# Optimization experiments

Hardware: AMD Instinct MI355X
Metric: run time of the kernel (lower is better)

Reference implementation:

```python
import jax, jax.numpy as jnp
import numpy as np

# ---- fixed problem dims (match init_kwargs) ----
B = 256            # graph pairs
NQ, NC = 96, 120   # nodes per query / corpus graph
EQ, EC = 192, 240  # edges per query / corpus graph
M = 256            # max_edge_set_size (pad target)
RAW = 32           # raw node/edge feature dim
H = 64             # node_state_dim
MSG = 128          # message_dim == encoded edge dim
SDIM = 64          # sinkhorn_feature_dim
PROP_STEPS = 3
TIME_STEPS = 2
SINK_ITERS = 10
TEMP = 0.1
N_NODES = B * (NQ + NC)
N_EDGES = B * (EQ + EC)


def _mlp2(x, W1, b1, W2, b2):
    return jax.nn.relu(x @ W1 + b1) @ W2 + b2


def _split_and_stack(ef):
    # edges laid out [q0, c0, q1, c1, ...]; pad each graph's edges to M
    D = ef.shape[-1]
    ef = ef.reshape(B, EQ + EC, D)
    q = jnp.pad(ef[:, :EQ], ((0, 0), (0, M - EQ), (0, 0)))
    c = jnp.pad(ef[:, EQ:], ((0, 0), (0, M - EC), (0, 0)))
    return q, c


def _sinkhorn(log_alpha):
    la = log_alpha / TEMP
    for _ in range(SINK_ITERS):
        la = la - jax.nn.logsumexp(la, axis=2, keepdims=True)
        la = la - jax.nn.logsumexp(la, axis=1, keepdims=True)
    return jnp.exp(la)


def setup_inputs() -> dict:
    key = jax.random.key(0)
    ks = jax.random.split(key, 16)
    rng = np.random.default_rng(0)
    nodes_per_graph = np.tile(np.array([NQ, NC]), B)            # [2B]
    node_offsets = np.concatenate([[0], np.cumsum(nodes_per_graph)[:-1]])
    edges_per_graph = np.tile(np.array([EQ, EC]), B)
    eg = np.repeat(np.arange(2 * B), edges_per_graph)           # graph id per edge
    from_idx = node_offsets[eg] + rng.integers(0, nodes_per_graph[eg])
    to_idx = node_offsets[eg] + rng.integers(0, nodes_per_graph[eg])

    def lin(k, i, o):
        return (jax.random.normal(k, (i, o), jnp.float32) / np.sqrt(i)).astype(jnp.float32)

    return {
        "node_features": jax.random.normal(ks[0], (N_NODES, RAW), jnp.float32),
        "edge_features": jax.random.normal(ks[1], (N_EDGES, RAW), jnp.float32),
        "from_idx": jnp.asarray(from_idx, jnp.int32),
        "to_idx": jnp.asarray(to_idx, jnp.int32),
        "enc_node_W": lin(ks[2], RAW, H), "enc_node_b": jnp.zeros((H,), jnp.float32),
        "enc_edge_W": lin(ks[3], RAW, MSG), "enc_edge_b": jnp.zeros((MSG,), jnp.float32),
        "msg_W1": lin(ks[4], 2 * H + MSG, 2 * MSG), "msg_b1": jnp.zeros((2 * MSG,), jnp.float32),
        "msg_W2": lin(ks[5], 2 * MSG, MSG), "msg_b2": jnp.zeros((MSG,), jnp.float32),
        "upd_W1": lin(ks[6], H + 2 * MSG, 2 * H), "upd_b1": jnp.zeros((2 * H,), jnp.float32),
        "upd_W2": lin(ks[7], 2 * H, H), "upd_b2": jnp.zeros((H,), jnp.float32),
        "int_W1": lin(ks[8], 2 * MSG, 2 * MSG), "int_b1": jnp.zeros((2 * MSG,), jnp.float32),
        "int_W2": lin(ks[9], 2 * MSG, MSG), "int_b2": jnp.zeros((MSG,), jnp.float32),
        "sink_W1": lin(ks[10], MSG, SDIM), "sink_b1": jnp.zeros((SDIM,), jnp.float32),
        "sink_W2": lin(ks[11], SDIM, SDIM), "sink_b2": jnp.zeros((SDIM,), jnp.float32),
    }


def _forward(node_features, edge_features,
             enc_node_W, enc_node_b, enc_edge_W, enc_edge_b,
             msg_W1, msg_b1, msg_W2, msg_b2,
             upd_W1, upd_b1, upd_W2, upd_b2,
             int_W1, int_b1, int_W2, int_b2,
             sink_W1, sink_b1, sink_W2, sink_b2,
             from_idx, to_idx):
    h0 = node_features @ enc_node_W + enc_node_b      # GraphEncoder (nodes)
    e0 = edge_features @ enc_edge_W + enc_edge_b      # GraphEncoder (edges) -> MSG dim
    mask_q = (jnp.arange(M) < EQ).astype(h0.dtype)[None, :, None]
    mask_c = (jnp.arange(M) < EC).astype(h0.dtype)[None, :, None]

    def edge_msgs(h, comb):
        hf, ht = h[from_idx], h[to_idx]
        mf = _mlp2(jnp.concatenate([hf, ht, comb], -1), msg_W1, msg_b1, msg_W2, msg_b2)
        mb = _mlp2(jnp.concatenate([ht, hf, comb], -1), msg_W1, msg_b1, msg_W2, msg_b2)
        return mf, mb

    plan = None
    q_store = c_store = None
    for _ in range(TIME_STEPS):
        h, e = h0, e0
        inter = jnp.zeros((N_EDGES, MSG), e0.dtype)
        for _ in range(PROP_STEPS):
            # interaction encoder on [edge_features_enc, interaction_features]
            comb = _mlp2(jnp.concatenate([e, inter], -1), int_W1, int_b1, int_W2, int_b2)
            # prop_layer: bidirectional messages + aggregation + node update
            mf, mb = edge_msgs(h, comb)
            agg_f = jax.ops.segment_sum(mf, to_idx, num_segments=N_NODES)
            agg_b = jax.ops.segment_sum(mb, from_idx, num_segments=N_NODES)
            h = _mlp2(jnp.concatenate([h, agg_f, agg_b], -1), upd_W1, upd_b1, upd_W2, upd_b2)
            # propagation_messages: per-edge messages from updated node states
            mf2, mb2 = edge_msgs(h, comb)
            e = mf2 + mb2
            # interaction features via transport-plan gather (zeros on first time step)
            if plan is None:
                inter = jnp.zeros((N_EDGES, MSG), e.dtype)
            else:
                qs, cs = _split_and_stack(e)
                q_int = jnp.einsum('bqc,bcd->bqd', plan, cs)[:, :EQ]
                c_int = jnp.einsum('bqc,bqd->bcd', plan, qs)[:, :EC]
                inter = jnp.concatenate([q_int, c_int], 1).reshape(N_EDGES, MSG)
        q_store, c_store = _split_and_stack(e)
        fq = _mlp2(q_store, sink_W1, sink_b1, sink_W2, sink_b2) * mask_q
        fc = _mlp2(c_store, sink_W1, sink_b1, sink_W2, sink_b2) * mask_c
        plan = _sinkhorn(jnp.einsum('bqd,bcd->bqc', fq, fc))
    # feature_alignment_score: -||Q - P C||_1 per pair
    return -jnp.abs(q_store - jnp.einsum('bqc,bcd->bqd', plan, c_store)).sum((1, 2))


def reference(node_features, edge_features, from_idx, to_idx,
              enc_node_W, enc_node_b, enc_edge_W, enc_edge_b,
              msg_W1, msg_b1, msg_W2, msg_b2,
              upd_W1, upd_b1, upd_W2, upd_b2,
              int_W1, int_b1, int_W2, int_b2,
              sink_W1, sink_b1, sink_W2, sink_b2):
    return _forward(node_features, edge_features,
                    enc_node_W, enc_node_b, enc_edge_W, enc_edge_b,
                    msg_W1, msg_b1, msg_W2, msg_b2,
                    upd_W1, upd_b1, upd_W2, upd_b2,
                    int_W1, int_b1, int_W2, int_b2,
                    sink_W1, sink_b1, sink_W2, sink_b2,
                    from_idx, to_idx)
```

## Files before the change

### kernel.cpp

```cpp
#include <hip/hip_runtime.h>
#include <math.h>

constexpr int BATCH = 256;
constexpr int EQ_   = 192;
constexpr int EC_   = 240;
constexpr int EPG   = 432;
constexpr int NPG   = 216;
constexpr int NN    = BATCH * NPG;
constexpr int NE    = BATCH * EPG;

typedef __attribute__((ext_vector_type(8))) short short8;
typedef __attribute__((ext_vector_type(4))) float floatx4;
typedef unsigned short u16;

__device__ __forceinline__ u16 f2bf(float x) {
  union { float f; unsigned u; } c; c.f = x;
  const unsigned r = (c.u + 0x7FFFu + ((c.u >> 16) & 1u)) >> 16;
  return (u16)r;
}
__device__ __forceinline__ float bf2f(u16 x) {
  union { unsigned u; float f; } c; c.u = ((unsigned)x) << 16;
  return c.f;
}
__device__ __forceinline__ unsigned pack2(float a, float b) {
  return (unsigned)f2bf(a) | ((unsigned)f2bf(b) << 16);
}
__device__ __forceinline__ short8 cvt8(const float* __restrict__ p) {
  const float4 a = *(const float4*)p;
  const float4 b = *(const float4*)(p + 4);
  short8 o;
  o[0]=(short)f2bf(a.x); o[1]=(short)f2bf(a.y); o[2]=(short)f2bf(a.z); o[3]=(short)f2bf(a.w);
  o[4]=(short)f2bf(b.x); o[5]=(short)f2bf(b.y); o[6]=(short)f2bf(b.z); o[7]=(short)f2bf(b.w);
  return o;
}

__device__ __forceinline__ void lse_online(float& m, float& s, float tt) {
  if (tt > m) { s = s * __expf(m - tt) + 1.f; m = tt; }
  else        { s += __expf(tt - m); }
}

__global__ __launch_bounds__(256)
void wconv(const float* __restrict__ W, u16* __restrict__ out, int K, int N)
{
  const int i = blockIdx.x * 256 + threadIdx.x;
  if (i < K * N) {
    const int n = i / K, k = i - n * K;
    out[i] = f2bf(W[(size_t)k * N + n]);
  }
}

__global__ __launch_bounds__(256)
void wconv_split(const float* __restrict__ W, u16* __restrict__ hi,
                 u16* __restrict__ lo, int K, int N)
{
  const int i = blockIdx.x * 256 + threadIdx.x;
  if (i < K * N) {
    const int n = i / K, k = i - n * K;
    const float w = W[(size_t)k * N + n];
    const u16 h = f2bf(w);
    hi[i] = h;
    lo[i] = f2bf(w - bf2f(h));
  }
}

template<int K1, int HID, int NOUT, int IN_MODE, int DUAL, int OUT_MODE, int WAVES>
__global__ __launch_bounds__(WAVES * 64, 4)
void mlp_mfma(const void* __restrict__ X, const void* __restrict__ P2,
              const void* __restrict__ P3, const u16* __restrict__ CB,
              const int* __restrict__ IA, const int* __restrict__ IB,
              const u16* __restrict__ W1t, const float* __restrict__ B1,
              const u16* __restrict__ W2t, const float* __restrict__ B2,
              float* __restrict__ Yf, u16* __restrict__ Yb0, u16* __restrict__ Yb1)
{
  constexpr int RT  = 32;
  constexpr int THREADS = WAVES * 64;
  constexpr int KCH = K1 / 8;
  constexpr int NT1 = HID / (WAVES * 16);
  constexpr int NT2 = (NOUT / (WAVES * 16) > 0) ? NOUT / (WAVES * 16) : 1;
  constexpr int SAB = RT * K1 * 2;
  constexpr int SHB = RT * (HID + 8) * 2;
  __shared__ __align__(16) char smem[(SAB > SHB ? SAB : SHB)];
  u16* sA = (u16*)smem;
  u16* sH = (u16*)smem;

  const int tid = threadIdx.x;
  const int rowBase = blockIdx.x * RT;

  for (int ch = tid; ch < RT * KCH; ch += THREADS) {
    const int r = ch / KCH, kc = ch - r * KCH;
    const int gr = rowBase + r, k0 = kc * 8;
    short8 pk;
    if constexpr (IN_MODE == 4) {
      const float* Xf  = (const float*)X;
      const float* P2f = (const float*)P2;
      if (k0 < 128)      pk = cvt8(&Xf[(size_t)gr * 128 + k0]);
      else if (P2f)      pk = cvt8(&P2f[(size_t)gr * 128 + (k0 - 128)]);
      else { pk = short8{0,0,0,0,0,0,0,0}; }
    } else if constexpr (IN_MODE == 1) {
      const u16* Hb = (const u16*)X;
      if (k0 < 64)       pk = *(const short8*)&Hb[(size_t)IA[gr] * 64 + k0];
      else if (k0 < 128) pk = *(const short8*)&Hb[(size_t)IB[gr] * 64 + (k0 - 64)];
      else               pk = *(const short8*)&CB[(size_t)gr * 128 + (k0 - 128)];
    } else {
      const u16* Hb = (const u16*)X;
      const u16* A0 = (const u16*)P2;
      const u16* A1 = (const u16*)P3;
      if (k0 < 64)       pk = *(const short8*)&Hb[(size_t)gr * 64 + k0];
      else if (k0 < 192) pk = *(const short8*)&A0[(size_t)gr * 128 + (k0 - 64)];
      else               pk = *(const short8*)&A1[(size_t)gr * 128 + (k0 - 192)];
    }
    const int byte = ((r * K1 + k0) * 2) ^ ((r & 7) << 4);
    *(short8*)((char*)sA + byte) = pk;
  }
  __syncthreads();

  const int wid = tid >> 6, lane = tid & 63;
  const int l15 = lane & 15, lg = lane >> 4;

  floatx4 acc1[1 + DUAL][2][NT1];
  #pragma unroll
  for (int d = 0; d <= DUAL; ++d)
    #pragma unroll
    for (int m = 0; m < 2; ++m)
      #pragma unroll
      for (int n = 0; n < NT1; ++n) acc1[d][m][n] = floatx4{0.f,0.f,0.f,0.f};

  #pragma unroll 2
  for (int kk = 0; kk < K1 / 32; ++kk) {
    short8 bw[NT1];
    #pragma unroll
    for (int n = 0; n < NT1; ++n) {
      const int col = wid * (HID / WAVES) + n * 16 + l15;
      bw[n] = *(const short8*)&W1t[(size_t)col * K1 + kk * 32 + lg * 8];
    }
    #pragma unroll
    for (int d = 0; d <= DUAL; ++d) {
      int k0 = kk * 32 + lg * 8;
      if (DUAL && d && k0 < 128) k0 ^= 64;
      #pragma unroll
      for (int m = 0; m < 2; ++m) {
        const int r = m * 16 + l15;
        const int byte = ((r * K1 + k0) * 2) ^ ((r & 7) << 4);
        const short8 af = *(const short8*)((char*)sA + byte);
        #pragma unroll
        for (int n = 0; n < NT1; ++n)
          acc1[d][m][n] = __builtin_amdgcn_mfma_f32_16x16x32_bf16(af, bw[n], acc1[d][m][n], 0, 0, 0);
      }
    }
  }
  __syncthreads();

  floatx4 accO[2][NT2];
  #pragma unroll
  for (int m = 0; m < 2; ++m)
    #pragma unroll
    for (int n = 0; n < NT2; ++n) accO[m][n] = floatx4{0.f,0.f,0.f,0.f};

  #pragma unroll
  for (int d = 0; d <= DUAL; ++d) {
    #pragma unroll
    for (int n = 0; n < NT1; ++n) {
      const int col = wid * (HID / WAVES) + n * 16 + l15;
      const float b1 = B1[col];
      #pragma unroll
      for (int m = 0; m < 2; ++m)
        #pragma unroll
        for (int r = 0; r < 4; ++r) {
          const int row = m * 16 + lg * 4 + r;
          const float y = acc1[d][m][n][r] + b1;
          sH[row * (HID + 8) + col] = f2bf(y > 0.f ? y : 0.f);
        }
    }
    __syncthreads();
    if (OUT_MODE == 2 && d == 1) {
      #pragma unroll
      for (int m = 0; m < 2; ++m)
        #pragma unroll
        for (int n = 0; n < NT2; ++n) accO[m][n] = floatx4{0.f,0.f,0.f,0.f};
    }
    #pragma unroll 2
    for (int kk = 0; kk < HID / 32; ++kk) {
      short8 bw2[NT2];
      #pragma unroll
      for (int n = 0; n < NT2; ++n) {
        const int col = wid * (NOUT / WAVES) + n * 16 + l15;
        bw2[n] = *(const short8*)&W2t[(size_t)col * HID + kk * 32 + lg * 8];
      }
      #pragma unroll
      for (int m = 0; m < 2; ++m) {
        const short8 af = *(const short8*)&sH[(m * 16 + l15) * (HID + 8) + kk * 32 + lg * 8];
        #pragma unroll
        for (int n = 0; n < NT2; ++n)
          accO[m][n] = __builtin_amdgcn_mfma_f32_16x16x32_bf16(af, bw2[n], accO[m][n], 0, 0, 0);
      }
    }
    if constexpr (OUT_MODE == 2) {
      u16* Y = d ? Yb1 : Yb0;
      #pragma unroll
      for (int n = 0; n < NT2; ++n) {
        const int col = wid * (NOUT / WAVES) + n * 16 + l15;
        const float b2 = B2[col];
        #pragma unroll
        for (int m = 0; m < 2; ++m)
          #pragma unroll
          for (int r = 0; r < 4; ++r) {
            const int gr = rowBase + m * 16 + lg * 4 + r;
            Y[(size_t)gr * NOUT + col] = f2bf(accO[m][n][r] + b2);
          }
      }
    }
    if (DUAL && d == 0) __syncthreads();
  }

  if constexpr (OUT_MODE != 2) {
    #pragma unroll
    for (int n = 0; n < NT2; ++n) {
      const int col = wid * (NOUT / WAVES) + n * 16 + l15;
      const float b2 = B2[col] * (float)(1 + DUAL);
      #pragma unroll
      for (int m = 0; m < 2; ++m)
        #pragma unroll
        for (int r = 0; r < 4; ++r) {
          const int gr = rowBase + m * 16 + lg * 4 + r;
          const float y = accO[m][n][r] + b2;
          if constexpr (OUT_MODE == 1) {
            Yb0[(size_t)gr * NOUT + col] = f2bf(y);
          } else {
            Yf[(size_t)gr * NOUT + col] = y;
            if constexpr (OUT_MODE == 3)
              Yb0[(size_t)gr * NOUT + col] = f2bf(y);
          }
        }
    }
  }
}

template<int EBF16>
__global__ __launch_bounds__(512, 4)
void comb_msg_fused(const void* __restrict__ E, const u16* __restrict__ INTER,
                    const u16* __restrict__ Hb,
                    const int* __restrict__ IA, const int* __restrict__ IB,
                    const u16* __restrict__ Wi1, const float* __restrict__ Bi1,
                    const u16* __restrict__ Wi2, const float* __restrict__ Bi2,
                    const u16* __restrict__ Wm1, const float* __restrict__ Bm1,
                    const u16* __restrict__ Wm2, const float* __restrict__ Bm2,
                    u16* __restrict__ COMB, u16* __restrict__ MI)
{
  constexpr int RT = 32;
  __shared__ __align__(16) char smem[RT * (256 + 8) * 2];
  u16* sA = (u16*)smem;
  u16* sH = (u16*)smem;

  const int tid = threadIdx.x;
  const int rowBase = blockIdx.x * RT;
  const int wid = tid >> 6, lane = tid & 63;
  const int l15 = lane & 15, lg = lane >> 4;

  for (int ch = tid; ch < RT * 32; ch += 512) {
    const int r = ch >> 5, kc = ch & 31;
    const int gr = rowBase + r, k0 = kc * 8;
    short8 pk;
    if (k0 < 128) {
      if constexpr (EBF16) pk = *(const short8*)&((const u16*)E)[(size_t)gr * 128 + k0];
      else                 pk = cvt8(&((const float*)E)[(size_t)gr * 128 + k0]);
    }
    else if (INTER) pk = *(const short8*)&INTER[(size_t)gr * 128 + (k0 - 128)];
    else            pk = short8{0,0,0,0,0,0,0,0};
    const int byte = ((r * 256 + k0) * 2) ^ ((r & 7) << 4);
    *(short8*)((char*)sA + byte) = pk;
  }
  __syncthreads();

  floatx4 c1[2][2];
  #pragma unroll
  for (int m = 0; m < 2; ++m) { c1[m][0] = floatx4{0,0,0,0}; c1[m][1] = floatx4{0,0,0,0}; }
  #pragma unroll 2
  for (int kk = 0; kk < 8; ++kk) {
    short8 bw[2];
    #pragma unroll
    for (int n = 0; n < 2; ++n) {
      const int col = wid * 32 + n * 16 + l15;
      bw[n] = *(const short8*)&Wi1[(size_t)col * 256 + kk * 32 + lg * 8];
    }
    #pragma unroll
    for (int m = 0; m < 2; ++m) {
      const int r = m * 16 + l15;
      const int byte = ((r * 256 + kk * 32 + lg * 8) * 2) ^ ((r & 7) << 4);
      const short8 af = *(const short8*)((char*)sA + byte);
      c1[m][0] = __builtin_amdgcn_mfma_f32_16x16x32_bf16(af, bw[0], c1[m][0], 0, 0, 0);
      c1[m][1] = __builtin_amdgcn_mfma_f32_16x16x32_bf16(af, bw[1], c1[m][1], 0, 0, 0);
    }
  }
  __syncthreads();
  #pragma unroll
  for (int n = 0; n < 2; ++n) {
    const int col = wid * 32 + n * 16 + l15;
    const float b1 = Bi1[col];
    #pragma unroll
    for (int m = 0; m < 2; ++m)
      #pragma unroll
      for (int r = 0; r < 4; ++r) {
        const int row = m * 16 + lg * 4 + r;
        const float y = c1[m][n][r] + b1;
        sH[row * 264 + col] = f2bf(y > 0.f ? y : 0.f);
      }
  }
  __syncthreads();
  floatx4 cO[2];
  cO[0] = floatx4{0,0,0,0}; cO[1] = floatx4{0,0,0,0};
  #pragma unroll 2
  for (int kk = 0; kk < 8; ++kk) {
    const int col = wid * 16 + l15;
    const short8 bw2 = *(const short8*)&Wi2[(size_t)col * 256 + kk * 32 + lg * 8];
    #pragma unroll
    for (int m = 0; m < 2; ++m) {
      const short8 af = *(const short8*)&sH[(m * 16 + l15) * 264 + kk * 32 + lg * 8];
      cO[m] = __builtin_amdgcn_mfma_f32_16x16x32_bf16(af, bw2, cO[m], 0, 0, 0);
    }
  }
  __syncthreads();

  {
    const int col = wid * 16 + l15;
    const float b2 = Bi2[col];
    #pragma unroll
    for (int m = 0; m < 2; ++m)
      #pragma unroll
      for (int r = 0; r < 4; ++r) {
        const int row = m * 16 + lg * 4 + r;
        const int gr = rowBase + row;
        const u16 v = f2bf(cO[m][r] + b2);
        COMB[(size_t)gr * 128 + col] = v;
        const int k0 = 128 + col;
        const int byte = ((row * 256 + k0) * 2) ^ ((row & 7) << 4);
        *(u16*)((char*)sA + byte) = v;
      }
  }
  for (int ch = tid; ch < RT * 16; ch += 512) {
    const int r = ch >> 4, kc = ch & 15;
    const int gr = rowBase + r, k0 = kc * 8;
    short8 pk;
    if (k0 < 64) pk = *(const short8*)&Hb[(size_t)IA[gr] * 64 + k0];
    else         pk = *(const short8*)&Hb[(size_t)IB[gr] * 64 + (k0 - 64)];
    const int byte = ((r * 256 + k0) * 2) ^ ((r & 7) << 4);
    *(short8*)((char*)sA + byte) = pk;
  }
  __syncthreads();

  floatx4 m1[2][2][2];
  #pragma unroll
  for (int d = 0; d < 2; ++d)
    #pragma unroll
    for (int m = 0; m < 2; ++m) { m1[d][m][0] = floatx4{0,0,0,0}; m1[d][m][1] = floatx4{0,0,0,0}; }
  #pragma unroll 2
  for (int kk = 0; kk < 8; ++kk) {
    short8 bw[2];
    #pragma unroll
    for (int n = 0; n < 2; ++n) {
      const int col = wid * 32 + n * 16 + l15;
      bw[n] = *(const short8*)&Wm1[(size_t)col * 256 + kk * 32 + lg * 8];
    }
    #pragma unroll
    for (int d = 0; d < 2; ++d) {
      int k0 = kk * 32 + lg * 8;
      if (d && k0 < 128) k0 ^= 64;
      #pragma unroll
      for (int m = 0; m < 2; ++m) {
        const int r = m * 16 + l15;
        const int byte = ((r * 256 + k0) * 2) ^ ((r & 7) << 4);
        const short8 af = *(const short8*)((char*)sA + byte);
        m1[d][m][0] = __builtin_amdgcn_mfma_f32_16x16x32_bf16(af, bw[0], m1[d][m][0], 0, 0, 0);
        m1[d][m][1] = __builtin_amdgcn_mfma_f32_16x16x32_bf16(af, bw[1], m1[d][m][1], 0, 0, 0);
      }
    }
  }
  __syncthreads();

  floatx4 mO[2];
  #pragma unroll
  for (int d = 0; d < 2; ++d) {
    #pragma unroll
    for (int n = 0; n < 2; ++n) {
      const int col = wid * 32 + n * 16 + l15;
      const float b1 = Bm1[col];
      #pragma unroll
      for (int m = 0; m < 2; ++m)
        #pragma unroll
        for (int r = 0; r < 4; ++r) {
          const int row = m * 16 + lg * 4 + r;
          const float y = m1[d][m][n][r] + b1;
          sH[row * 264 + col] = f2bf(y > 0.f ? y : 0.f);
        }
    }
    __syncthreads();
    mO[0] = floatx4{0,0,0,0}; mO[1] = floatx4{0,0,0,0};
    #pragma unroll 2
    for (int kk = 0; kk < 8; ++kk) {
      const int col = wid * 16 + l15;
      const short8 bw2 = *(const short8*)&Wm2[(size_t)col * 256 + kk * 32 + lg * 8];
      #pragma unroll
      for (int m = 0; m < 2; ++m) {
        const short8 af = *(const short8*)&sH[(m * 16 + l15) * 264 + kk * 32 + lg * 8];
        mO[m] = __builtin_amdgcn_mfma_f32_16x16x32_bf16(af, bw2, mO[m], 0, 0, 0);
      }
    }
    {
      const int col = wid * 16 + l15;
      const float b2 = Bm2[col];
      #pragma unroll
      for (int m = 0; m < 2; ++m)
        #pragma unroll
        for (int r = 0; r < 4; ++r) {
          const int gr = rowBase + m * 16 + lg * 4 + r;
          MI[(size_t)gr * 256 + d * 128 + col] = f2bf(mO[m][r] + b2);
        }
    }
    if (d == 0) __syncthreads();
  }
}

__global__ __launch_bounds__(512)
void scatter_agg(const u16* __restrict__ MI,
                 const int* __restrict__ FI, const int* __restrict__ TI,
                 u16* __restrict__ AggF, u16* __restrict__ AggB)
{
  const int pair = blockIdx.x >> 1, dir = blockIdx.x & 1;
  const int* SI = dir ? FI : TI;
  u16* Agg      = dir ? AggB : AggF;
  const int tid = threadIdx.x;
  __shared__ float sAgg[NPG * 128];

  for (int i = tid; i < NPG * 128; i += 512) sAgg[i] = 0.f;
  __syncthreads();

  for (int i = tid; i < EPG * 32; i += 512) {
    const int edge = i >> 5, cb = i & 31;
    const int er = pair * EPG + edge;
    const int node = SI[er] - pair * NPG;
    const size_t base = (size_t)er * 256 + dir * 128 + cb;
    #pragma unroll
    for (int k = 0; k < 4; ++k)
      atomicAdd(&sAgg[node * 128 + cb + 32 * k], bf2f(MI[base + 32 * k]));
  }
  __syncthreads();
  unsigned* dst = (unsigned*)(Agg + (size_t)pair * NPG * 128);
  for (int i = tid; i < NPG * 64; i += 512)
    dst[i] = pack2(sAgg[2 * i], sAgg[2 * i + 1]);
}

template<int K1, int HID, int NOUT, int IN_MODE, int SINGLE, int OUTBF>
__global__ __launch_bounds__(256)
void fused_mlp(const float* __restrict__ X, const float* __restrict__ P1,
               const float* __restrict__ W1, const float* __restrict__ B1,
               const float* __restrict__ W2, const float* __restrict__ B2,
               float* __restrict__ Y, u16* __restrict__ Yb, int maskLen)
{
  constexpr int RT = 32, BK = 32;
  constexpr int J1 = HID / 32;
  constexpr int J2 = NOUT / 32;
  constexpr int BMAX = (HID > NOUT ? HID : NOUT);
  __shared__ float sA[RT * 33];
  __shared__ float sB[BK * BMAX];
  __shared__ float sH[SINGLE ? 1 : RT * (HID + 1)];

  const int t  = threadIdx.x;
  const int tx = t & 31, ty = t >> 5;
  const int rowBase = blockIdx.x * RT;

  float acc[4][J1];
  #pragma unroll
  for (int i = 0; i < 4; ++i)
    #pragma unroll
    for (int j = 0; j < J1; ++j) acc[i][j] = 0.f;

  for (int kb = 0; kb < K1; kb += BK) {
    for (int l = t; l < RT * BK; l += 256) {
      const int r = l >> 5, k = l & 31;
      const int gr = rowBase + r, gk = kb + k;
      float v;
      if constexpr (IN_MODE == 0) {
        v = X[(size_t)gr * K1 + gk];
      } else {
        const int bb = gr >> 8, m = gr & 255;
        constexpr int off = (IN_MODE == 5) ? 0 : EQ_;
        constexpr int len = (IN_MODE == 5) ? EQ_ : EC_;
        v = (m < len) ? P1[((size_t)bb * EPG + off + m) * 128 + gk] : 0.f;
      }
      sA[r * 33 + k] = v;
    }
    for (int l = t * 4; l < BK * HID; l += 1024) {
      *(float4*)&sB[l] = *(const float4*)&W1[(size_t)(kb + l / HID) * HID + (l % HID)];
    }
    __syncthreads();
    #pragma unroll
    for (int k = 0; k < BK; ++k) {
      const float a0 = sA[(ty*4+0)*33+k], a1 = sA[(ty*4+1)*33+k],
                  a2 = sA[(ty*4+2)*33+k], a3 = sA[(ty*4+3)*33+k];
      #pragma unroll
      for (int j = 0; j < J1; ++j) {
        const float bb = sB[k * HID + tx + 32*j];
        acc[0][j] += a0 * bb; acc[1][j] += a1 * bb;
        acc[2][j] += a2 * bb; acc[3][j] += a3 * bb;
      }
    }
    __syncthreads();
  }

  if constexpr (SINGLE) {
    #pragma unroll
    for (int j = 0; j < J1; ++j) {
      const int col = tx + 32*j;
      const float bias = B1[col];
      #pragma unroll
      for (int i = 0; i < 4; ++i) {
        const int gr = rowBase + ty*4 + i;
        if constexpr (OUTBF) Yb[(size_t)gr * HID + col] = f2bf(acc[i][j] + bias);
        else                 Y[(size_t)gr * HID + col] = acc[i][j] + bias;
      }
    }
  }
}

template<int OFFSET, int LEN>
__global__ __launch_bounds__(256)
void sink_mlp_split(const float* __restrict__ E,
                    const u16* __restrict__ W1hi, const u16* __restrict__ W1lo,
                    const float* __restrict__ B1,
                    const u16* __restrict__ W2hi, const u16* __restrict__ W2lo,
                    const float* __restrict__ B2,
                    float* __restrict__ Y)
{
  __shared__ u16 sAhi[32 * 136], sAlo[32 * 136];
  __shared__ u16 sHhi[32 * 72],  sHlo[32 * 72];
  const int tid = threadIdx.x;
  const int rowBase = blockIdx.x * 32;

  for (int ch = tid; ch < 32 * 16; ch += 256) {
    const int r = ch >> 4, kc = ch & 15;
    const int gr = rowBase + r, k0 = kc * 8;
    const int b = gr >> 8, m = gr & 255;
    short8 hi, lo;
    if (m < LEN) {
      const float* src = &E[((size_t)b * EPG + OFFSET + m) * 128 + k0];
      #pragma unroll
      for (int j = 0; j < 8; ++j) {
        const float v = src[j];
        const u16 h = f2bf(v);
        hi[j] = (short)h;
        lo[j] = (short)f2bf(v - bf2f(h));
      }
    } else {
      hi = short8{0,0,0,0,0,0,0,0};
      lo = short8{0,0,0,0,0,0,0,0};
    }
    *(short8*)&sAhi[r * 136 + k0] = hi;
    *(short8*)&sAlo[r * 136 + k0] = lo;
  }
  __syncthreads();

  const int wid = tid >> 6, lane = tid & 63;
  const int l15 = lane & 15, lg = lane >> 4;
  const int col = wid * 16 + l15;

  floatx4 acc[2];
  acc[0] = floatx4{0,0,0,0}; acc[1] = floatx4{0,0,0,0};
  #pragma unroll
  for (int kk = 0; kk < 4; ++kk) {
    const short8 bh = *(const short8*)&W1hi[(size_t)col * 128 + kk * 32 + lg * 8];
    const short8 bl = *(const short8*)&W1lo[(size_t)col * 128 + kk * 32 + lg * 8];
    #pragma unroll
    for (int m = 0; m < 2; ++m) {
      const int r = m * 16 + l15;
      const short8 ahi = *(const short8*)&sAhi[r * 136 + kk * 32 + lg * 8];
      const short8 alo = *(const short8*)&sAlo[r * 136 + kk * 32 + lg * 8];
      acc[m] = __builtin_amdgcn_mfma_f32_16x16x32_bf16(ahi, bh, acc[m], 0, 0, 0);
      acc[m] = __builtin_amdgcn_mfma_f32_16x16x32_bf16(ahi, bl, acc[m], 0, 0, 0);
      acc[m] = __builtin_amdgcn_mfma_f32_16x16x32_bf16(alo, bh, acc[m], 0, 0, 0);
    }
  }
  {
    const float b1 = B1[col];
    #pragma unroll
    for (int m = 0; m < 2; ++m)
      #pragma unroll
      for (int r4 = 0; r4 < 4; ++r4) {
        const int row = m * 16 + lg * 4 + r4;
        float y = acc[m][r4] + b1;
        y = y > 0.f ? y : 0.f;
        const u16 h = f2bf(y);
        sHhi[row * 72 + col] = h;
        sHlo[row * 72 + col] = f2bf(y - bf2f(h));
      }
  }
  __syncthreads();
  floatx4 acc2[2];
  acc2[0] = floatx4{0,0,0,0}; acc2[1] = floatx4{0,0,0,0};
  #pragma unroll
  for (int kk = 0; kk < 2; ++kk) {
    const short8 bh = *(const short8*)&W2hi[(size_t)col * 64 + kk * 32 + lg * 8];
    const short8 bl = *(const short8*)&W2lo[(size_t)col * 64 + kk * 32 + lg * 8];
    #pragma unroll
    for (int m = 0; m < 2; ++m) {
      const int r = m * 16 + l15;
      const short8 ahi = *(const short8*)&sHhi[r * 72 + kk * 32 + lg * 8];
      const short8 alo = *(const short8*)&sHlo[r * 72 + kk * 32 + lg * 8];
      acc2[m] = __builtin_amdgcn_mfma_f32_16x16x32_bf16(ahi, bh, acc2[m], 0, 0, 0);
      acc2[m] = __builtin_amdgcn_mfma_f32_16x16x32_bf16(ahi, bl, acc2[m], 0, 0, 0);
      acc2[m] = __builtin_amdgcn_mfma_f32_16x16x32_bf16(alo, bh, acc2[m], 0, 0, 0);
    }
  }
  {
    const float b2 = B2[col];
    #pragma unroll
    for (int m = 0; m < 2; ++m)
      #pragma unroll
      for (int r4 = 0; r4 < 4; ++r4) {
        const int gr = rowBase + m * 16 + lg * 4 + r4;
        float y = acc2[m][r4] + b2;
        if ((gr & 255) >= LEN) y = 0.f;
        Y[(size_t)gr * 64 + col] = y;
      }
  }
}

__global__ __launch_bounds__(256)
void gemm_nt_scale(const float* __restrict__ A, const float* __restrict__ Bm,
                   float* __restrict__ C, float scale)
{
  const int b = blockIdx.z, qt = blockIdx.x, ct = blockIdx.y;
  __shared__ float sA[64 * 68];
  __shared__ float sB[64 * 68];
  const int t = threadIdx.x;
  const int tx = t & 15, ty = t >> 4;
  const float* Ab = A  + (size_t)b * 16384 + (size_t)qt * 4096;
  const float* Bb = Bm + (size_t)b * 16384 + (size_t)ct * 4096;
  for (int l = t * 4; l < 64 * 64; l += 1024) {
    const int r = l >> 6, d = l & 63;
    *(float4*)&sA[r*68 + d] = *(const float4*)&Ab[r*64 + d];
    *(float4*)&sB[r*68 + d] = *(const float4*)&Bb[r*64 + d];
  }
  __syncthreads();
  float acc[4][4] = {};
  #pragma unroll
  for (int d = 0; d < 64; ++d) {
    float a[4], bb[4];
    #pragma unroll
    for (int i = 0; i < 4; ++i) a[i]  = sA[(ty*4+i)*68 + d];
    #pragma unroll
    for (int j = 0; j < 4; ++j) bb[j] = sB[(tx+16*j)*68 + d];
    #pragma unroll
    for (int i = 0; i < 4; ++i)
      #pragma unroll
      for (int j = 0; j < 4; ++j) acc[i][j] += a[i] * bb[j];
  }
  float* Cb = C + (size_t)b * 65536 + (size_t)(qt*64) * 256 + ct*64;
  #pragma unroll
  for (int i = 0; i < 4; ++i)
    #pragma unroll
    for (int j = 0; j < 4; ++j)
      Cb[(ty*4+i)*256 + tx + 16*j] = acc[i][j] * scale;
}

template<int TRANSA, int EBF16, int OUTBF>
__global__ __launch_bounds__(256)
void gemm_plan_mfma(const float* __restrict__ P, const void* __restrict__ E,
                    void* __restrict__ Y, int RPB, int YOFF, int VOFF,
                    int VLEN, int maskRows)
{
  __shared__ u16 sP[64 * 40];
  __shared__ u16 sVT[128 * 40];
  const int b = blockIdx.y, rt = blockIdx.x;
  const int t = threadIdx.x;
  const int wid = t >> 6, lane = t & 63;
  const int l15 = lane & 15, lg = lane >> 4;
  const float* Pb = P + (size_t)b * 65536;

  floatx4 acc[8];
  #pragma unroll
  for (int n = 0; n < 8; ++n) acc[n] = floatx4{0.f,0.f,0.f,0.f};

  for (int kb = 0; kb < 256; kb += 32) {
    if constexpr (TRANSA == 0) {
      for (int l = t; l < 64 * 32; l += 256) {
        const int r = l >> 5, k = l & 31;
        sP[r * 40 + k] = f2bf(Pb[(size_t)(rt * 64 + r) * 256 + kb + k]);
      }
    } else {
      for (int l = t; l < 64 * 32; l += 256) {
        const int q = l >> 6, c = l & 63;
        sP[c * 40 + q] = f2bf(Pb[(size_t)(kb + q) * 256 + rt * 64 + c]);
      }
    }
    for (int l = t; l < 32 * 128; l += 256) {
      const int k = l >> 7, d = l & 127;
      const int vr = kb + k;
      u16 v = 0;
      if (vr < VLEN) {
        if constexpr (EBF16) v = ((const u16*)E)[((size_t)b * EPG + VOFF + vr) * 128 + d];
        else                 v = f2bf(((const float*)E)[((size_t)b * EPG + VOFF + vr) * 128 + d]);
      }
      sVT[d * 40 + k] = v;
    }
    __syncthreads();
    const short8 af = *(const short8*)&sP[(wid * 16 + l15) * 40 + lg * 8];
    #pragma unroll
    for (int n = 0; n < 8; ++n) {
      const short8 bw = *(const short8*)&sVT[(n * 16 + l15) * 40 + lg * 8];
      acc[n] = __builtin_amdgcn_mfma_f32_16x16x32_bf16(af, bw, acc[n], 0, 0, 0);
    }
    __syncthreads();
  }
  #pragma unroll
  for (int n = 0; n < 8; ++n) {
    const int col = n * 16 + l15;
    #pragma unroll
    for (int r = 0; r < 4; ++r) {
      const int row = rt * 64 + wid * 16 + lg * 4 + r;
      if (row < maskRows) {
        const size_t idx = ((size_t)b * RPB + YOFF + row) * 128 + col;
        if constexpr (OUTBF) ((u16*)Y)[idx] = f2bf(acc[n][r]);
        else                 ((float*)Y)[idx] = acc[n][r];
      }
    }
  }
}

__global__ __launch_bounds__(1024)
void sinkhorn_fused(float* __restrict__ S)
{
  const int b = blockIdx.x, t = threadIdx.x;
  float* Sb = S + (size_t)b * 65536;
  const int w = t >> 6, lane = t & 63;
  const int cbase = lane * 4;
  __shared__ float ps[16 * 256];
  __shared__ float su[256], sv[256];
  if (t < 256) sv[t] = 0.f;
  __syncthreads();

  for (int it = 0; it < 10; ++it) {
    const float4 v4 = *(const float4*)&sv[cbase];
    float4 cs = {0.f, 0.f, 0.f, 0.f};
    #pragma unroll 2
    for (int i = 0; i < 16; ++i) {
      const int r = w * 16 + i;
      const float4 s4 = *(const float4*)&Sb[(size_t)r * 256 + cbase];
      const float ax = s4.x + v4.x, ay = s4.y + v4.y;
      const float az = s4.z + v4.z, aw = s4.w + v4.w;
      float m = fmaxf(fmaxf(ax, ay), fmaxf(az, aw));
      #pragma unroll
      for (int off = 32; off; off >>= 1) m = fmaxf(m, __shfl_xor(m, off));
      float s = __expf(ax - m) + __expf(ay - m) + __expf(az - m) + __expf(aw - m);
      #pragma unroll
      for (int off = 32; off; off >>= 1) s += __shfl_xor(s, off);
      const float u = -(m + __logf(s));
      if (lane == 0) su[r] = u;
      cs.x += __expf(s4.x + u);
      cs.y += __expf(s4.y + u);
      cs.z += __expf(s4.z + u);
      cs.w += __expf(s4.w + u);
    }
    *(float4*)&ps[w * 256 + cbase] = cs;
    __syncthreads();
    if (t < 256) {
      float s = 0.f;
      #pragma unroll
      for (int k = 0; k < 16; ++k) s += ps[k * 256 + t];
      sv[t] = -__logf(fmaxf(s, 1e-38f));
    }
    __syncthreads();
  }
  for (int i = t; i < 16384; i += 1024) {
    const int row = i >> 6, c4 = (i & 63) * 4;
    float4 s4 = *(float4*)&Sb[(size_t)row * 256 + c4];
    const float uu = su[row];
    const float4 v4 = *(const float4*)&sv[c4];
    s4.x = __expf(s4.x + uu + v4.x);
    s4.y = __expf(s4.y + uu + v4.y);
    s4.z = __expf(s4.z + uu + v4.z);
    s4.w = __expf(s4.w + uu + v4.w);
    *(float4*)&Sb[(size_t)row * 256 + c4] = s4;
  }
}

__global__ __launch_bounds__(256)
void escore_kernel(const float* __restrict__ e, const float* __restrict__ pc,
                   float* __restrict__ out)
{
  const int b = blockIdx.x, t = threadIdx.x;
  float acc = 0.f;
  for (int i4 = t; i4 < 8192; i4 += 256) {
    const int flat = i4 * 4;
    const int m = flat >> 7, d = flat & 127;
    float4 p = *(const float4*)&pc[((size_t)b * 256 + m) * 128 + d];
    float4 q = {0.f, 0.f, 0.f, 0.f};
    if (m < EQ_) q = *(const float4*)&e[((size_t)b * EPG + m) * 128 + d];
    acc += fabsf(q.x - p.x) + fabsf(q.y - p.y) + fabsf(q.z - p.z) + fabsf(q.w - p.w);
  }
  __shared__ float red[256];
  red[t] = acc; __syncthreads();
  for (int s2 = 128; s2 > 0; s2 >>= 1) { if (t < s2) red[t] += red[t + s2]; __syncthreads(); }
  if (t == 0) out[b] = -red[0];
}

extern "C" void kernel_launch(void* const* d_in, const int* in_sizes, int n_in,
                              void* d_out, int out_size, void* d_ws, size_t ws_size,
                              hipStream_t stream)
{
  const float* node_features = (const float*)d_in[0];
  const float* edge_features = (const float*)d_in[1];
  const int*   from_idx      = (const int*)d_in[2];
  const int*   to_idx        = (const int*)d_in[3];
  const float* enc_node_W = (const float*)d_in[4];
  const float* enc_node_b = (const float*)d_in[5];
  const float* enc_edge_W = (const float*)d_in[6];
  const float* enc_edge_b = (const float*)d_in[7];
  const float* msg_W1 = (const float*)d_in[8];
  const float* msg_b1 = (const float*)d_in[9];
  const float* msg_W2 = (const float*)d_in[10];
  const float* msg_b2 = (const float*)d_in[11];
  const float* upd_W1 = (const float*)d_in[12];
  const float* upd_b1 = (const float*)d_in[13];
  const float* upd_W2 = (const float*)d_in[14];
  const float* upd_b2 = (const float*)d_in[15];
  const float* int_W1 = (const float*)d_in[16];
  const float* int_b1 = (const float*)d_in[17];
  const float* int_W2 = (const float*)d_in[18];
  const float* int_b2 = (const float*)d_in[19];
  const float* sink_W1 = (const float*)d_in[20];
  const float* sink_b1 = (const float*)d_in[21];
  const float* sink_W2 = (const float*)d_in[22];
  const float* sink_b2 = (const float*)d_in[23];
  float* out = (float*)d_out;

  u16* wsu = (u16*)d_ws;
  u16*   hb  = wsu;
  float* e   = (float*)(wsu + (size_t)NN * 64);
  float* shr = e + (size_t)NE * 128;
  float* S   = shr + (size_t)BATCH * 32768;
  u16* comb  = (u16*)(S + (size_t)BATCH * 65536);
  u16* e1b   = comb + (size_t)NE * 128;
  u16* h1b   = e1b + (size_t)NE * 128;
  u16* wi1 = h1b + (size_t)NN * 64;
  u16* wi2 = wi1 + 65536;
  u16* wm1 = wi2 + 32768;
  u16* wm2 = wm1 + 65536;
  u16* wu1 = wm2 + 32768;
  u16* wu2 = wu1 + 40960;
  u16* ws1h = wu2 + 8192;
  u16* ws1l = ws1h + 8192;
  u16* ws2h = ws1l + 8192;
  u16* ws2l = ws2h + 4096;

  u16* mI = (u16*)e;
  u16* interb = (u16*)shr;
  u16* aggFb  = (u16*)shr;
  u16* aggBb  = aggFb + (size_t)NN * 128;
  float* fq   = shr;
  float* fc   = shr + (size_t)BATCH * 16384;
  float* pc   = shr;

  wconv<<<256, 256, 0, stream>>>(int_W1, wi1, 256, 256);
  wconv<<<128, 256, 0, stream>>>(int_W2, wi2, 256, 128);
  wconv<<<256, 256, 0, stream>>>(msg_W1, wm1, 256, 256);
  wconv<<<128, 256, 0, stream>>>(msg_W2, wm2, 256, 128);
  wconv<<<160, 256, 0, stream>>>(upd_W1, wu1, 320, 128);
  wconv<<< 32, 256, 0, stream>>>(upd_W2, wu2, 128, 64);
  wconv_split<<<32, 256, 0, stream>>>(sink_W1, ws1h, ws1l, 128, 64);
  wconv_split<<<16, 256, 0, stream>>>(sink_W2, ws2h, ws2l, 64, 64);

  fused_mlp<32,64,64,0,1,1><<<NN/32, 256, 0, stream>>>(
      node_features, nullptr, enc_node_W, enc_node_b, nullptr, nullptr,
      nullptr, hb, -1);
  fused_mlp<32,128,128,0,1,0><<<NE/32, 256, 0, stream>>>(
      edge_features, nullptr, enc_edge_W, enc_edge_b, nullptr, nullptr,
      e, nullptr, -1);

  for (int p = 0; p < 3; ++p) {
    comb_msg_fused<0><<<NE/32, 512, 0, stream>>>(
        e, nullptr, hb, from_idx, to_idx,
        wi1, int_b1, wi2, int_b2, wm1, msg_b1, wm2, msg_b2, comb, mI);
    scatter_agg<<<BATCH*2, 512, 0, stream>>>(mI, from_idx, to_idx, aggFb, aggBb);
    mlp_mfma<320,128,64,3,0,1,4><<<NN/32, 256, 0, stream>>>(
        hb, aggFb, aggBb, nullptr, nullptr, nullptr,
        wu1, upd_b1, wu2, upd_b2, nullptr, hb, nullptr);
    if (p == 0) {
      hipMemcpyAsync(h1b, hb, (size_t)NN * 64 * 2, hipMemcpyDeviceToDevice, stream);
      mlp_mfma<256,256,128,1,1,3,8><<<NE/32, 512, 0, stream>>>(
          hb, nullptr, nullptr, comb, from_idx, to_idx,
          wm1, msg_b1, wm2, msg_b2, e, e1b, nullptr);
    } else {
      mlp_mfma<256,256,128,1,1,0,8><<<NE/32, 512, 0, stream>>>(
          hb, nullptr, nullptr, comb, from_idx, to_idx,
          wm1, msg_b1, wm2, msg_b2, e, nullptr, nullptr);
    }
  }
  sink_mlp_split<0,   EQ_><<<BATCH*8, 256, 0, stream>>>(
      e, ws1h, ws1l, sink_b1, ws2h, ws2l, sink_b2, fq);
  sink_mlp_split<EQ_, EC_><<<BATCH*8, 256, 0, stream>>>(
      e, ws1h, ws1l, sink_b1, ws2h, ws2l, sink_b2, fc);
  gemm_nt_scale<<<dim3(4,4,BATCH), 256, 0, stream>>>(fq, fc, S, 10.0f);
  sinkhorn_fused<<<BATCH, 1024, 0, stream>>>(S);

  hipMemcpyAsync(hb, h1b, (size_t)NN * 64 * 2, hipMemcpyDeviceToDevice, stream);
  gemm_plan_mfma<0,1,1><<<dim3(4, BATCH), 256, 0, stream>>>(
      S, e1b, interb, EPG, 0,   EQ_, EC_, EQ_);
  gemm_plan_mfma<1,1,1><<<dim3(4, BATCH), 256, 0, stream>>>(
      S, e1b, interb, EPG, EQ_, 0,   EQ_, EC_);

  comb_msg_fused<1><<<NE/32, 512, 0, stream>>>(
      e1b, interb, hb, from_idx, to_idx,
      wi1, int_b1, wi2, int_b2, wm1, msg_b1, wm2, msg_b2, comb, mI);
  scatter_agg<<<BATCH*2, 512, 0, stream>>>(mI, from_idx, to_idx, aggFb, aggBb);
  mlp_mfma<320,128,64,3,0,1,4><<<NN/32, 256, 0, stream>>>(
      hb, aggFb, aggBb, nullptr, nullptr, nullptr,
      wu1, upd_b1, wu2, upd_b2, nullptr, hb, nullptr);
  mlp_mfma<256,256,128,1,1,0,8><<<NE/32, 512, 0, stream>>>(
      hb, nullptr, nullptr, comb, from_idx, to_idx,
      wm1, msg_b1, wm2, msg_b2, e, nullptr, nullptr);
  gemm_plan_mfma<0,0,1><<<dim3(4, BATCH), 256, 0, stream>>>(
      S, e, interb, EPG, 0,   EQ_, EC_, EQ_);
  gemm_plan_mfma<1,0,1><<<dim3(4, BATCH), 256, 0, stream>>>(
      S, e, interb, EPG, EQ_, 0,   EQ_, EC_);

  comb_msg_fused<0><<<NE/32, 512, 0, stream>>>(
      e, interb, hb, from_idx, to_idx,
      wi1, int_b1, wi2, int_b2, wm1, msg_b1, wm2, msg_b2, comb, mI);
  scatter_agg<<<BATCH*2, 512, 0, stream>>>(mI, from_idx, to_idx, aggFb, aggBb);
  mlp_mfma<320,128,64,3,0,1,4><<<NN/32, 256, 0, stream>>>(
      hb, aggFb, aggBb, nullptr, nullptr, nullptr,
      wu1, upd_b1, wu2, upd_b2, nullptr, hb, nullptr);
  mlp_mfma<256,256,128,1,1,0,8><<<NE/32, 512, 0, stream>>>(
      hb, nullptr, nullptr, comb, from_idx, to_idx,
      wm1, msg_b1, wm2, msg_b2, e, nullptr, nullptr);

  sink_mlp_split<0,   EQ_><<<BATCH*8, 256, 0, stream>>>(
      e, ws1h, ws1l, sink_b1, ws2h, ws2l, sink_b2, fq);
  sink_mlp_split<EQ_, EC_><<<BATCH*8, 256, 0, stream>>>(
      e, ws1h, ws1l, sink_b1, ws2h, ws2l, sink_b2, fc);
  gemm_nt_scale<<<dim3(4,4,BATCH), 256, 0, stream>>>(fq, fc, S, 10.0f);
  sinkhorn_fused<<<BATCH, 1024, 0, stream>>>(S);

  gemm_plan_mfma<0,0,0><<<dim3(4, BATCH), 256, 0, stream>>>(
      S, e, pc, 256, 0, EQ_, EC_, 256);
  escore_kernel<<<BATCH, 256, 0, stream>>>(e, pc, out);
}
```

Baseline: 3.271 ms.

## Split scatter aggregation by channel half, use split-bf16 MFMA for score GEMM, bf16 edge encoder

The scatter aggregation kernel now splits each direction's 128 channels into two 64-channel halves across separate blocks. That halves shared memory per block, with padding to reduce bank conflicts, and doubles the block count for better occupancy. The fp32 FMA score GEMM is replaced by a bf16 hi/lo split MFMA version that keeps near-fp32 accuracy on matrix cores. The edge encoder now writes bf16 directly into e1b, and the first propagation step reads that bf16 buffer, which cuts fp32 traffic. The split-bf16 product drops the lo*lo term, a small precision risk. Unused code in fused_mlp is removed.

```diff
diff --git a/kernel.cpp b/kernel.cpp
--- a/kernel.cpp
+++ b/kernel.cpp
@@ -424,28 +424,30 @@
                  const int* __restrict__ FI, const int* __restrict__ TI,
                  u16* __restrict__ AggF, u16* __restrict__ AggB)
 {
-  const int pair = blockIdx.x >> 1, dir = blockIdx.x & 1;
+  const int pair = blockIdx.x >> 2, dir = (blockIdx.x >> 1) & 1, half = blockIdx.x & 1;
   const int* SI = dir ? FI : TI;
   u16* Agg      = dir ? AggB : AggF;
   const int tid = threadIdx.x;
-  __shared__ float sAgg[NPG * 128];
-
-  for (int i = tid; i < NPG * 128; i += 512) sAgg[i] = 0.f;
-  __syncthreads();
-
-  for (int i = tid; i < EPG * 32; i += 512) {
-    const int edge = i >> 5, cb = i & 31;
+  __shared__ float sAgg[NPG * 65];
+
+  for (int i = tid; i < NPG * 65; i += 512) sAgg[i] = 0.f;
+  __syncthreads();
+
+  for (int i = tid; i < EPG * 16; i += 512) {
+    const int edge = i >> 4, c0 = i & 15;
     const int er = pair * EPG + edge;
     const int node = SI[er] - pair * NPG;
-    const size_t base = (size_t)er * 256 + dir * 128 + cb;
+    const size_t base = (size_t)er * 256 + dir * 128 + half * 64 + c0;
     #pragma unroll
     for (int k = 0; k < 4; ++k)
-      atomicAdd(&sAgg[node * 128 + cb + 32 * k], bf2f(MI[base + 32 * k]));
-  }
-  __syncthreads();
-  unsigned* dst = (unsigned*)(Agg + (size_t)pair * NPG * 128);
-  for (int i = tid; i < NPG * 64; i += 512)
-    dst[i] = pack2(sAgg[2 * i], sAgg[2 * i + 1]);
+      atomicAdd(&sAgg[node * 65 + c0 + 16 * k], bf2f(MI[base + 16 * k]));
+  }
+  __syncthreads();
+  for (int i = tid; i < NPG * 32; i += 512) {
+    const int node = i >> 5, cp = i & 31;
+    unsigned* dst = (unsigned*)(Agg + (size_t)(pair * NPG + node) * 128 + half * 64);
+    dst[cp] = pack2(sAgg[node * 65 + 2 * cp], sAgg[node * 65 + 2 * cp + 1]);
+  }
 }
 
 template<int K1, int HID, int NOUT, int IN_MODE, int SINGLE, int OUTBF>
@@ -457,11 +459,9 @@
 {
   constexpr int RT = 32, BK = 32;
   constexpr int J1 = HID / 32;
-  constexpr int J2 = NOUT / 32;
-  constexpr int BMAX = (HID > NOUT ? HID : NOUT);
+  constexpr int BMAX = HID;
   __shared__ float sA[RT * 33];
   __shared__ float sB[BK * BMAX];
-  __shared__ float sH[SINGLE ? 1 : RT * (HID + 1)];
 
   const int t  = threadIdx.x;
   const int tx = t & 31, ty = t >> 5;
@@ -477,15 +477,7 @@
     for (int l = t; l < RT * BK; l += 256) {
       const int r = l >> 5, k = l & 31;
       const int gr = rowBase + r, gk = kb + k;
-      float v;
-      if constexpr (IN_MODE == 0) {
-        v = X[(size_t)gr * K1 + gk];
-      } else {
-        const int bb = gr >> 8, m = gr & 255;
-        constexpr int off = (IN_MODE == 5) ? 0 : EQ_;
-        constexpr int len = (IN_MODE == 5) ? EQ_ : EC_;
-        v = (m < len) ? P1[((size_t)bb * EPG + off + m) * 128 + gk] : 0.f;
-      }
+      float v = X[(size_t)gr * K1 + gk];
       sA[r * 33 + k] = v;
     }
     for (int l = t * 4; l < BK * HID; l += 1024) {
@@ -506,17 +498,15 @@
     __syncthreads();
   }
 
-  if constexpr (SINGLE) {
-    #pragma unroll
-    for (int j = 0; j < J1; ++j) {
-      const int col = tx + 32*j;
-      const float bias = B1[col];
-      #pragma unroll
-      for (int i = 0; i < 4; ++i) {
-        const int gr = rowBase + ty*4 + i;
-        if constexpr (OUTBF) Yb[(size_t)gr * HID + col] = f2bf(acc[i][j] + bias);
-        else                 Y[(size_t)gr * HID + col] = acc[i][j] + bias;
-      }
+  #pragma unroll
+  for (int j = 0; j < J1; ++j) {
+    const int col = tx + 32*j;
+    const float bias = B1[col];
+    #pragma unroll
+    for (int i = 0; i < 4; ++i) {
+      const int gr = rowBase + ty*4 + i;
+      if constexpr (OUTBF) Yb[(size_t)gr * HID + col] = f2bf(acc[i][j] + bias);
+      else                 Y[(size_t)gr * HID + col] = acc[i][j] + bias;
     }
   }
 }
@@ -624,41 +614,59 @@
 }
 
 __global__ __launch_bounds__(256)
-void gemm_nt_scale(const float* __restrict__ A, const float* __restrict__ Bm,
+void gemm_nt_split(const float* __restrict__ A, const float* __restrict__ Bm,
                    float* __restrict__ C, float scale)
 {
+  __shared__ u16 sQh[64 * 72], sQl[64 * 72];
+  __shared__ u16 sCh[64 * 72], sCl[64 * 72];
   const int b = blockIdx.z, qt = blockIdx.x, ct = blockIdx.y;
-  __shared__ float sA[64 * 68];
-  __shared__ float sB[64 * 68];
   const int t = threadIdx.x;
-  const int tx = t & 15, ty = t >> 4;
   const float* Ab = A  + (size_t)b * 16384 + (size_t)qt * 4096;
   const float* Bb = Bm + (size_t)b * 16384 + (size_t)ct * 4096;
-  for (int l = t * 4; l < 64 * 64; l += 1024) {
-    const int r = l >> 6, d = l & 63;
-    *(float4*)&sA[r*68 + d] = *(const float4*)&Ab[r*64 + d];
-    *(float4*)&sB[r*68 + d] = *(const float4*)&Bb[r*64 + d];
-  }
-  __syncthreads();
-  float acc[4][4] = {};
-  #pragma unroll
-  for (int d = 0; d < 64; ++d) {
-    float a[4], bb[4];
-    #pragma unroll
-    for (int i = 0; i < 4; ++i) a[i]  = sA[(ty*4+i)*68 + d];
-    #pragma unroll
-    for (int j = 0; j < 4; ++j) bb[j] = sB[(tx+16*j)*68 + d];
-    #pragma unroll
-    for (int i = 0; i < 4; ++i)
-      #pragma unroll
-      for (int j = 0; j < 4; ++j) acc[i][j] += a[i] * bb[j];
-  }
-  float* Cb = C + (size_t)b * 65536 + (size_t)(qt*64) * 256 + ct*64;
-  #pragma unroll
-  for (int i = 0; i < 4; ++i)
-    #pragma unroll
-    for (int j = 0; j < 4; ++j)
-      Cb[(ty*4+i)*256 + tx + 16*j] = acc[i][j] * scale;
+
+  for (int i = t; i < 64 * 64; i += 256) {
+    const int r = i >> 6, d = i & 63;
+    float v = Ab[r * 64 + d];
+    u16 h = f2bf(v);
+    sQh[r * 72 + d] = h;
+    sQl[r * 72 + d] = f2bf(v - bf2f(h));
+    v = Bb[r * 64 + d];
+    h = f2bf(v);
+    sCh[r * 72 + d] = h;
+    sCl[r * 72 + d] = f2bf(v - bf2f(h));
+  }
+  __syncthreads();
+
+  const int wid = t >> 6, lane = t & 63;
+  const int l15 = lane & 15, lg = lane >> 4;
+
+  floatx4 acc[4];
+  #pragma unroll
+  for (int n = 0; n < 4; ++n) acc[n] = floatx4{0.f,0.f,0.f,0.f};
+
+  #pragma unroll
+  for (int kk = 0; kk < 2; ++kk) {
+    const short8 ahi = *(const short8*)&sQh[(wid * 16 + l15) * 72 + kk * 32 + lg * 8];
+    const short8 alo = *(const short8*)&sQl[(wid * 16 + l15) * 72 + kk * 32 + lg * 8];
+    #pragma unroll
+    for (int n = 0; n < 4; ++n) {
+      const short8 bh = *(const short8*)&sCh[(n * 16 + l15) * 72 + kk * 32 + lg * 8];
+      const short8 bl = *(const short8*)&sCl[(n * 16 + l15) * 72 + kk * 32 + lg * 8];
+      acc[n] = __builtin_amdgcn_mfma_f32_16x16x32_bf16(ahi, bh, acc[n], 0, 0, 0);
+      acc[n] = __builtin_amdgcn_mfma_f32_16x16x32_bf16(ahi, bl, acc[n], 0, 0, 0);
+      acc[n] = __builtin_amdgcn_mfma_f32_16x16x32_bf16(alo, bh, acc[n], 0, 0, 0);
+    }
+  }
+  float* Cb = C + (size_t)b * 65536;
+  #pragma unroll
+  for (int n = 0; n < 4; ++n) {
+    const int col = ct * 64 + n * 16 + l15;
+    #pragma unroll
+    for (int r4 = 0; r4 < 4; ++r4) {
+      const int row = qt * 64 + wid * 16 + lg * 4 + r4;
+      Cb[(size_t)row * 256 + col] = acc[n][r4] * scale;
+    }
+  }
 }
 
 template<int TRANSA, int EBF16, int OUTBF>
@@ -871,15 +879,20 @@
   fused_mlp<32,64,64,0,1,1><<<NN/32, 256, 0, stream>>>(
       node_features, nullptr, enc_node_W, enc_node_b, nullptr, nullptr,
       nullptr, hb, -1);
-  fused_mlp<32,128,128,0,1,0><<<NE/32, 256, 0, stream>>>(
+  fused_mlp<32,128,128,0,1,1><<<NE/32, 256, 0, stream>>>(
       edge_features, nullptr, enc_edge_W, enc_edge_b, nullptr, nullptr,
-      e, nullptr, -1);
+      nullptr, e1b, -1);
 
   for (int p = 0; p < 3; ++p) {
-    comb_msg_fused<0><<<NE/32, 512, 0, stream>>>(
-        e, nullptr, hb, from_idx, to_idx,
-        wi1, int_b1, wi2, int_b2, wm1, msg_b1, wm2, msg_b2, comb, mI);
-    scatter_agg<<<BATCH*2, 512, 0, stream>>>(mI, from_idx, to_idx, aggFb, aggBb);
+    if (p == 0)
+      comb_msg_fused<1><<<NE/32, 512, 0, stream>>>(
+          e1b, nullptr, hb, from_idx, to_idx,
+          wi1, int_b1, wi2, int_b2, wm1, msg_b1, wm2, msg_b2, comb, mI);
+    else
+      comb_msg_fused<0><<<NE/32, 512, 0, stream>>>(
+          e, nullptr, hb, from_idx, to_idx,
+          wi1, int_b1, wi2, int_b2, wm1, msg_b1, wm2, msg_b2, comb, mI);
+    scatter_agg<<<BATCH*4, 512, 0, stream>>>(mI, from_idx, to_idx, aggFb, aggBb);
     mlp_mfma<320,128,64,3,0,1,4><<<NN/32, 256, 0, stream>>>(
         hb, aggFb, aggBb, nullptr, nullptr, nullptr,
         wu1, upd_b1, wu2, upd_b2, nullptr, hb, nullptr);
@@ -898,7 +911,7 @@
       e, ws1h, ws1l, sink_b1, ws2h, ws2l, sink_b2, fq);
   sink_mlp_split<EQ_, EC_><<<BATCH*8, 256, 0, stream>>>(
       e, ws1h, ws1l, sink_b1, ws2h, ws2l, sink_b2, fc);
-  gemm_nt_scale<<<dim3(4,4,BATCH), 256, 0, stream>>>(fq, fc, S, 10.0f);
+  gemm_nt_split<<<dim3(4,4,BATCH), 256, 0, stream>>>(fq, fc, S, 10.0f);
   sinkhorn_fused<<<BATCH, 1024, 0, stream>>>(S);
 
   hipMemcpyAsync(hb, h1b, (size_t)NN * 64 * 2, hipMemcpyDeviceToDevice, stream);
@@ -910,7 +923,7 @@
   comb_msg_fused<1><<<NE/32, 512, 0, stream>>>(
       e1b, interb, hb, from_idx, to_idx,
       wi1, int_b1, wi2, int_b2, wm1, msg_b1, wm2, msg_b2, comb, mI);
-  scatter_agg<<<BATCH*2, 512, 0, stream>>>(mI, from_idx, to_idx, aggFb, aggBb);
+  scatter_agg<<<BATCH*4, 512, 0, stream>>>(mI, from_idx, to_idx, aggFb, aggBb);
   mlp_mfma<320,128,64,3,0,1,4><<<NN/32, 256, 0, stream>>>(
       hb, aggFb, aggBb, nullptr, nullptr, nullptr,
       wu1, upd_b1, wu2, upd_b2, nullptr, hb, nullptr);
@@ -925,7 +938,7 @@
   comb_msg_fused<0><<<NE/32, 512, 0, stream>>>(
       e, interb, hb, from_idx, to_idx,
       wi1, int_b1, wi2, int_b2, wm1, msg_b1, wm2, msg_b2, comb, mI);
-  scatter_agg<<<BATCH*2, 512, 0, stream>>>(mI, from_idx, to_idx, aggFb, aggBb);
+  scatter_agg<<<BATCH*4, 512, 0, stream>>>(mI, from_idx, to_idx, aggFb, aggBb);
   mlp_mfma<320,128,64,3,0,1,4><<<NN/32, 256, 0, stream>>>(
       hb, aggFb, aggBb, nullptr, nullptr, nullptr,
       wu1, upd_b1, wu2, upd_b2, nullptr, hb, nullptr);
@@ -937,7 +950,7 @@
       e, ws1h, ws1l, sink_b1, ws2h, ws2l, sink_b2, fq);
   sink_mlp_split<EQ_, EC_><<<BATCH*8, 256, 0, stream>>>(
       e, ws1h, ws1l, sink_b1, ws2h, ws2l, sink_b2, fc);
-  gemm_nt_scale<<<dim3(4,4,BATCH), 256, 0, stream>>>(fq, fc, S, 10.0f);
+  gemm_nt_split<<<dim3(4,4,BATCH), 256, 0, stream>>>(fq, fc, S, 10.0f);
   sinkhorn_fused<<<BATCH, 1024, 0, stream>>>(S);
 
   gemm_plan_mfma<0,0,0><<<dim3(4, BATCH), 256, 0, stream>>>(
```

Measured after the change: 3.264 ms. About the same (-0.2%).
